# Optimization experiments

Measured on AMD Instinct MI355X. Metric: run time of the kernel, lower is better.

Reference implementation:

```python
import jax, jax.numpy as jnp
import numpy as np

LN_EPS = 1e-5
NORM_EPS = 1e-12


def entmax15_last(x):
    """Exact 1.5-entmax over the last axis (Peters & Martins sort algorithm)."""
    d = x.shape[-1]
    x = x / 2.0
    x = x - jnp.max(x, axis=-1, keepdims=True)
    xs = jnp.sort(x, axis=-1)[..., ::-1]  # descending
    k = jnp.arange(1, d + 1, dtype=x.dtype)
    mean = jnp.cumsum(xs, axis=-1) / k
    meansq = jnp.cumsum(xs * xs, axis=-1) / k
    ss = k * (meansq - jnp.square(mean))
    delta = (1.0 - ss) / k
    tau = mean - jnp.sqrt(jnp.clip(delta, 0.0))
    support = (tau <= xs).astype(jnp.int32)
    k_star = jnp.sum(support, axis=-1, keepdims=True) - 1  # last valid index
    tau_star = jnp.take_along_axis(tau, k_star, axis=-1)
    return jnp.square(jnp.maximum(x - tau_star, 0.0))


def layer_norm(x, gamma, beta):
    mu = jnp.mean(x, axis=-1, keepdims=True)
    var = jnp.mean(jnp.square(x - mu), axis=-1, keepdims=True)
    return (x - mu) / jnp.sqrt(var + LN_EPS) * gamma + beta


def setup_inputs() -> dict:
    key = jax.random.key(0)
    ks = jax.random.split(key, 4)
    B, M, N, D, T, L = 256, 64, 32, 128, 64, 128
    return {
        "x": jax.random.normal(ks[0], (B, M, D), dtype=jnp.float32),
        "route_weights": jax.random.normal(ks[1], (M, N, D, T), dtype=jnp.float32),
        "thread": jax.random.uniform(ks[2], (1, M, N), dtype=jnp.float32),
        "routing_leaves": jax.random.uniform(ks[3], (L, T), dtype=jnp.float32),
        "ln_gamma": jnp.ones((T,), dtype=jnp.float32),
        "ln_beta": jnp.zeros((T,), dtype=jnp.float32),
    }


def reference(x, route_weights, thread, routing_leaves, ln_gamma, ln_beta):
    # entmax15 over dim=-2 (the in_capsule_size axis D) of route_weights [M,N,D,T]
    w = jnp.swapaxes(route_weights, -1, -2)
    w = entmax15_last(w)
    weights = jnp.swapaxes(w, -1, -2)
    # priors: [B, M, N, T]
    priors = jnp.einsum('bmd,mndt->bmnt', x, weights)
    # routing
    leave_hash = routing_leaves / jnp.maximum(
        jnp.linalg.norm(routing_leaves, axis=-1, keepdims=True), NORM_EPS)
    votes = jax.nn.sigmoid(jnp.einsum('ld,bmnt->bmnl', leave_hash, priors)) if False else \
        jax.nn.sigmoid(jnp.einsum('ld,bmnd->bmnl', leave_hash, priors))  # [B,M,N,L]
    mean_cap = jnp.mean(votes, axis=1, keepdims=True)
    dis = jnp.mean(jnp.square(votes - mean_cap), axis=-1)  # [B,M,N]
    weight = jax.nn.relu(jnp.square(thread) - dis)
    prob = jax.nn.softmax(weight, axis=-2)  # over M (in capsules)
    next_caps = jnp.sum(prob[:, :, :, None] * priors, axis=1)  # [B,N,T]
    return layer_norm(next_caps, ln_gamma, ln_beta)
```

## Files before the change

### kernel.cpp

```cpp
#include <hip/hip_runtime.h>
#include <hip/hip_bf16.h>
#include <math.h>

#define B_ 256
#define M_ 64
#define N_ 32
#define D_ 128
#define T_ 64
#define L_ 128

typedef __attribute__((ext_vector_type(8))) short short8;
typedef __attribute__((ext_vector_type(4))) float floatx4;

__device__ __forceinline__ unsigned short f2bf(float f) {
  unsigned int u = __float_as_uint(f);
  unsigned int r = (u + 0x7fffu + ((u >> 16) & 1u)) >> 16;
  return (unsigned short)r;
}
__device__ __forceinline__ float bf2f(unsigned short s) {
  return __uint_as_float(((unsigned int)s) << 16);
}
__device__ __forceinline__ float frcp(float x) { return __builtin_amdgcn_rcpf(x); }
__device__ __forceinline__ unsigned pk2bf(float a, float b) {
  __hip_bfloat162 h = __float22bfloat162_rn(make_float2(a, b));
  unsigned u;
  __builtin_memcpy(&u, &h, 4);
  return u;
}

template <int CTRL>
__device__ __forceinline__ float dpp_f(float x) {
  return __int_as_float(__builtin_amdgcn_update_dpp(
      __float_as_int(x), __float_as_int(x), CTRL, 0xf, 0xf, false));
}
__device__ __forceinline__ float rsum16(float x) {
  x += dpp_f<0x121>(x);
  x += dpp_f<0x122>(x);
  x += dpp_f<0x124>(x);
  x += dpp_f<0x128>(x);
  return x;
}
__device__ __forceinline__ float rmax16(float x) {
  x = fmaxf(x, dpp_f<0x121>(x));
  x = fmaxf(x, dpp_f<0x122>(x));
  x = fmaxf(x, dpp_f<0x124>(x));
  x = fmaxf(x, dpp_f<0x128>(x));
  return x;
}

__global__ __launch_bounds__(256) void k_prep(const float* __restrict__ x,
                                              const float* __restrict__ leaves,
                                              unsigned short* __restrict__ xb2,
                                              unsigned short* __restrict__ lhn,
                                              const float* __restrict__ thr,
                                              float* __restrict__ thrT) {
  const int tid = threadIdx.x;
  const int bx = blockIdx.x;
  if (bx < 1024) {
    int idx = bx * 256 + tid;
    int j = idx & 15, b = (idx >> 4) & 255, m = idx >> 12;
    const float* xs = x + ((size_t)b * M_ + m) * D_ + j;
    float v[8];
#pragma unroll
    for (int i = 0; i < 8; ++i) v[i] = xs[i * 16];
    unsigned short* dst = xb2 + ((size_t)m * B_ + b) * D_ + j * 8;
    uint4 w;
    w.x = pk2bf(v[0], v[1]);
    w.y = pk2bf(v[2], v[3]);
    w.z = pk2bf(v[4], v[5]);
    w.w = pk2bf(v[6], v[7]);
    *(uint4*)dst = w;
  } else if (bx == 1024) {
    if (tid < L_) {
      const float* r = leaves + tid * T_;
      float ss = 0.f;
      for (int i = 0; i < T_; ++i) ss = fmaf(r[i], r[i], ss);
      float inv = frcp(fmaxf(sqrtf(ss), 1e-12f));
      unsigned short* o = lhn + tid * T_;
      for (int i = 0; i < T_; ++i) o[i] = f2bf(r[i] * inv);
    }
  } else {
#pragma unroll
    for (int k = 0; k < 8; ++k) {
      int idx = k * 256 + tid;
      int nn = idx >> 6, mm = idx & 63;
      thrT[idx] = thr[mm * N_ + nn];
    }
  }
}

#define BS_STRIDE 136
__global__ __launch_bounds__(256, 8) void k_wpriors(const unsigned short* __restrict__ xb2,
                                                    const float* __restrict__ rw,
                                                    unsigned short* __restrict__ priors) {
  const int m = blockIdx.x, n = blockIdx.y;
  const int tid = threadIdx.x;
  const int wid = tid >> 6, lane = tid & 63;
  const int row16 = lane & 15, quad = lane >> 4;

  __shared__ __align__(16) unsigned short Bs[64 * BS_STRIDE];

  {
    const int g = tid >> 4, j = tid & 15;
    const float* base = rw + (size_t)(m * N_ + n) * (D_ * T_) + g * 4;
    floatx4 xv[8];
#pragma unroll
    for (int i = 0; i < 8; ++i)
      xv[i] = *(const floatx4*)(base + (size_t)(i * 16 + j) * T_);

    floatx4 mx = xv[0];
#pragma unroll
    for (int i = 1; i < 8; ++i)
#pragma unroll
      for (int c = 0; c < 4; ++c) mx[c] = fmaxf(mx[c], xv[i][c]);
#pragma unroll
    for (int c = 0; c < 4; ++c) mx[c] = rmax16(mx[c]);
#pragma unroll
    for (int i = 0; i < 8; ++i)
#pragma unroll
      for (int c = 0; c < 4; ++c) xv[i][c] = (xv[i][c] - mx[c]) * 0.5f;

    floatx4 lo = (floatx4){-1.f, -1.f, -1.f, -1.f};
    floatx4 hi = (floatx4){0.f, 0.f, 0.f, 0.f};
    for (int it = 0; it < 8; ++it) {
      floatx4 tau, f = (floatx4){0.f, 0.f, 0.f, 0.f};
#pragma unroll
      for (int c = 0; c < 4; ++c) tau[c] = 0.5f * (lo[c] + hi[c]);
#pragma unroll
      for (int i = 0; i < 8; ++i)
#pragma unroll
        for (int c = 0; c < 4; ++c) {
          float u = fmaxf(xv[i][c] - tau[c], 0.0f);
          f[c] = fmaf(u, u, f[c]);
        }
#pragma unroll
      for (int c = 0; c < 4; ++c) f[c] = rsum16(f[c]);
#pragma unroll
      for (int c = 0; c < 4; ++c) {
        bool ge = f[c] >= 1.0f;
        lo[c] = ge ? tau[c] : lo[c];
        hi[c] = ge ? hi[c] : tau[c];
      }
    }
    floatx4 tau0, cnt = (floatx4){0,0,0,0}, s1 = (floatx4){0,0,0,0}, s2 = (floatx4){0,0,0,0};
#pragma unroll
    for (int c = 0; c < 4; ++c) tau0[c] = 0.5f * (lo[c] + hi[c]);
#pragma unroll
    for (int i = 0; i < 8; ++i)
#pragma unroll
      for (int c = 0; c < 4; ++c) {
        bool in = xv[i][c] > tau0[c];
        float q = in ? xv[i][c] : 0.0f;
        cnt[c] += in ? 1.0f : 0.0f;
        s1[c] += q;
        s2[c] = fmaf(q, q, s2[c]);
      }
#pragma unroll
    for (int c = 0; c < 4; ++c) {
      cnt[c] = rsum16(cnt[c]);
      s1[c] = rsum16(s1[c]);
      s2[c] = rsum16(s2[c]);
    }
    floatx4 tau;
#pragma unroll
    for (int c = 0; c < 4; ++c) {
      float rc = frcp(cnt[c]);
      float mean = s1[c] * rc;
      float ss = s2[c] - mean * s1[c];
      float delta = (1.0f - ss) * rc;
      tau[c] = mean - sqrtf(fmaxf(delta, 0.0f));
    }

#pragma unroll
    for (int c = 0; c < 4; ++c) {
      float u[8];
#pragma unroll
      for (int i = 0; i < 8; ++i) {
        float v = fmaxf(xv[i][c] - tau[c], 0.0f);
        u[i] = v * v;
      }
      uint4 w;
      w.x = pk2bf(u[0], u[1]);
      w.y = pk2bf(u[2], u[3]);
      w.z = pk2bf(u[4], u[5]);
      w.w = pk2bf(u[6], u[7]);
      *(uint4*)&Bs[(g * 4 + c) * BS_STRIDE + j * 8] = w;
    }
  }
  __syncthreads();

#pragma unroll
  for (int c = 0; c < 2; ++c) {
#pragma unroll
    for (int sub = 0; sub < 2; ++sub) {
      const int b = c * 128 + wid * 32 + sub * 16 + row16;
      const unsigned short* xptr = xb2 + ((size_t)m * B_ + b) * D_ + quad * 8;
      short8 xfr[4];
#pragma unroll
      for (int ks = 0; ks < 4; ++ks) xfr[ks] = *(const short8*)(xptr + ks * 32);

      floatx4 acc[4];
#pragma unroll
      for (int cf = 0; cf < 4; ++cf) acc[cf] = (floatx4){0.f, 0.f, 0.f, 0.f};
#pragma unroll
      for (int cf = 0; cf < 4; ++cf) {
        short8 afr[4];
#pragma unroll
        for (int ks = 0; ks < 4; ++ks)
          afr[ks] = *(const short8*)&Bs[(cf * 16 + row16) * BS_STRIDE + ks * 32 + quad * 8];
#pragma unroll
        for (int ks = 0; ks < 4; ++ks)
          acc[cf] = __builtin_amdgcn_mfma_f32_16x16x32_bf16(afr[ks], xfr[ks], acc[cf], 0, 0, 0);
      }

      unsigned X0x = pk2bf(acc[0][0], acc[0][1]), X0y = pk2bf(acc[0][2], acc[0][3]);
      unsigned X1x = pk2bf(acc[1][0], acc[1][1]), X1y = pk2bf(acc[1][2], acc[1][3]);
      unsigned X2x = pk2bf(acc[2][0], acc[2][1]), X2y = pk2bf(acc[2][2], acc[2][3]);
      unsigned X3x = pk2bf(acc[3][0], acc[3][1]), X3y = pk2bf(acc[3][2], acc[3][3]);

      const bool hi2 = (quad & 2) != 0;
      unsigned s0x = hi2 ? X0x : X2x, s0y = hi2 ? X0y : X2y;
      unsigned s1x = hi2 ? X1x : X3x, s1y = hi2 ? X1y : X3y;
      unsigned r0x = __shfl_xor(s0x, 32), r0y = __shfl_xor(s0y, 32);
      unsigned r1x = __shfl_xor(s1x, 32), r1y = __shfl_xor(s1y, 32);
      unsigned A0x = hi2 ? r0x : X0x, A0y = hi2 ? r0y : X0y;
      unsigned A1x = hi2 ? r1x : X1x, A1y = hi2 ? r1y : X1y;
      unsigned A2x = hi2 ? X2x : r0x, A2y = hi2 ? X2y : r0y;
      unsigned A3x = hi2 ? X3x : r1x, A3y = hi2 ? X3y : r1y;
      const bool odd = (quad & 1) != 0;
      unsigned t0x = odd ? A0x : A1x, t0y = odd ? A0y : A1y;
      unsigned t1x = odd ? A2x : A3x, t1y = odd ? A2y : A3y;
      unsigned u0x = __shfl_xor(t0x, 16), u0y = __shfl_xor(t0y, 16);
      unsigned u1x = __shfl_xor(t1x, 16), u1y = __shfl_xor(t1y, 16);
      uint4 w0, w1;
      w0.x = odd ? u0x : A0x;  w0.y = odd ? u0y : A0y;
      w0.z = odd ? A1x : u0x;  w0.w = odd ? A1y : u0y;
      w1.x = odd ? u1x : A2x;  w1.y = odd ? u1y : A2y;
      w1.z = odd ? A3x : u1x;  w1.w = odd ? A3y : u1y;

      unsigned short* dst = priors + (((size_t)n * B_ + b) * M_ + m) * T_ + quad * 16;
      *(uint4*)dst = w0;
      *(uint4*)(dst + 8) = w1;
    }
  }
}

__global__ __launch_bounds__(256, 4) void k_route(const unsigned short* __restrict__ priors,
                                                  const unsigned short* __restrict__ lhn,
                                                  const float* __restrict__ thrT,
                                                  const float* __restrict__ gamma,
                                                  const float* __restrict__ beta,
                                                  float* __restrict__ out) {
  const int n = blockIdx.x, g4 = blockIdx.y;
  const int tid = threadIdx.x;
  const int wid = tid >> 6, lane = tid & 63;
  const int col = lane & 15, quad = lane >> 4;

  __shared__ float probL[4][64];

  const int b = g4 * 4 + wid;

  const unsigned short* base = priors + ((size_t)n * B_ + b) * (M_ * T_);
  short8 afr[4][2];
#pragma unroll
  for (int mt = 0; mt < 4; ++mt)
#pragma unroll
    for (int ks = 0; ks < 2; ++ks)
      afr[mt][ks] = *(const short8*)(base + (mt * 16 + col) * T_ + ks * 32 + quad * 8);

  float thv = thrT[n * 64 + lane];

  float dis[4][4];
#pragma unroll
  for (int mt = 0; mt < 4; ++mt)
#pragma unroll
    for (int r = 0; r < 4; ++r) dis[mt][r] = 0.f;

#pragma unroll
  for (int s4 = 0; s4 < 4; ++s4) {
    floatx4 acc[4][2];
#pragma unroll
    for (int mt = 0; mt < 4; ++mt)
#pragma unroll
      for (int lt = 0; lt < 2; ++lt) acc[mt][lt] = (floatx4){0.f, 0.f, 0.f, 0.f};

#pragma unroll
    for (int lt = 0; lt < 2; ++lt) {
#pragma unroll
      for (int ks = 0; ks < 2; ++ks) {
        short8 bfr = *(const short8*)(lhn + (s4 * 32 + lt * 16 + col) * T_ + ks * 32 + quad * 8);
#pragma unroll
        for (int mt = 0; mt < 4; ++mt)
          acc[mt][lt] = __builtin_amdgcn_mfma_f32_16x16x32_bf16(afr[mt][ks], bfr, acc[mt][lt], 0, 0, 0);
      }
    }

#pragma unroll
    for (int mt = 0; mt < 4; ++mt)
#pragma unroll
      for (int lt = 0; lt < 2; ++lt)
#pragma unroll
        for (int r = 0; r < 4; ++r)
          acc[mt][lt][r] = frcp(1.0f + __expf(-acc[mt][lt][r]));

    float mc[2];
#pragma unroll
    for (int lt = 0; lt < 2; ++lt) {
      float s = 0.f;
#pragma unroll
      for (int mt = 0; mt < 4; ++mt)
#pragma unroll
        for (int r = 0; r < 4; ++r) s += acc[mt][lt][r];
      s += __shfl_xor(s, 16);
      s += __shfl_xor(s, 32);
      mc[lt] = s * (1.0f / 64.0f);
    }

#pragma unroll
    for (int mt = 0; mt < 4; ++mt)
#pragma unroll
      for (int r = 0; r < 4; ++r) {
        float s = 0.f;
#pragma unroll
        for (int lt = 0; lt < 2; ++lt) {
          float df = acc[mt][lt][r] - mc[lt];
          s = fmaf(df, df, s);
        }
        dis[mt][r] += s;
      }
  }

#pragma unroll
  for (int mt = 0; mt < 4; ++mt)
#pragma unroll
    for (int r = 0; r < 4; ++r) dis[mt][r] = rsum16(dis[mt][r]);

  float e[4][4];
  float mxw = 0.f;
#pragma unroll
  for (int mt = 0; mt < 4; ++mt)
#pragma unroll
    for (int r = 0; r < 4; ++r) {
      float th = __shfl(thv, mt * 16 + quad * 4 + r);
      float w = fmaxf(th * th - dis[mt][r] * (1.0f / 128.0f), 0.0f);
      e[mt][r] = w;
      mxw = fmaxf(mxw, w);
    }
  mxw = fmaxf(mxw, __shfl_xor(mxw, 16));
  mxw = fmaxf(mxw, __shfl_xor(mxw, 32));
  float ssum = 0.f;
#pragma unroll
  for (int mt = 0; mt < 4; ++mt)
#pragma unroll
    for (int r = 0; r < 4; ++r) {
      e[mt][r] = __expf(e[mt][r] - mxw);
      ssum += e[mt][r];
    }
  ssum += __shfl_xor(ssum, 16);
  ssum += __shfl_xor(ssum, 32);
  float inv = frcp(ssum);
  if (col == 0) {
#pragma unroll
    for (int mt = 0; mt < 4; ++mt)
#pragma unroll
      for (int r = 0; r < 4; ++r)
        probL[wid][mt * 16 + quad * 4 + r] = e[mt][r] * inv;
  }

  float pr[4];
#pragma unroll
  for (int mt = 0; mt < 4; ++mt) pr[mt] = probL[wid][mt * 16 + col];

  float o[2][8];
#pragma unroll
  for (int ks = 0; ks < 2; ++ks)
#pragma unroll
    for (int j = 0; j < 8; ++j) o[ks][j] = 0.f;
#pragma unroll
  for (int mt = 0; mt < 4; ++mt)
#pragma unroll
    for (int ks = 0; ks < 2; ++ks)
#pragma unroll
      for (int j = 0; j < 8; ++j)
        o[ks][j] = fmaf(pr[mt], bf2f((unsigned short)afr[mt][ks][j]), o[ks][j]);
#pragma unroll
  for (int ks = 0; ks < 2; ++ks)
#pragma unroll
    for (int j = 0; j < 8; ++j) o[ks][j] = rsum16(o[ks][j]);

  float mu = 0.f;
#pragma unroll
  for (int ks = 0; ks < 2; ++ks)
#pragma unroll
    for (int j = 0; j < 8; ++j) mu += o[ks][j];
  mu += __shfl_xor(mu, 16);
  mu += __shfl_xor(mu, 32);
  mu *= (1.0f / 64.0f);
  float var = 0.f;
#pragma unroll
  for (int ks = 0; ks < 2; ++ks)
#pragma unroll
    for (int j = 0; j < 8; ++j) {
      float d = o[ks][j] - mu;
      o[ks][j] = d;
      var = fmaf(d, d, var);
    }
  var += __shfl_xor(var, 16);
  var += __shfl_xor(var, 32);
  var *= (1.0f / 64.0f);
  float rstd = rsqrtf(var + 1e-5f);

  if (col == 0) {
    float* obase = out + ((size_t)b * N_ + n) * T_;
#pragma unroll
    for (int ks = 0; ks < 2; ++ks) {
      int tb = ks * 32 + quad * 8;
      float4 g0 = *(const float4*)(gamma + tb);
      float4 g1 = *(const float4*)(gamma + tb + 4);
      float4 b0 = *(const float4*)(beta + tb);
      float4 b1 = *(const float4*)(beta + tb + 4);
      float4 r0, r1;
      r0.x = o[ks][0] * rstd * g0.x + b0.x;
      r0.y = o[ks][1] * rstd * g0.y + b0.y;
      r0.z = o[ks][2] * rstd * g0.z + b0.z;
      r0.w = o[ks][3] * rstd * g0.w + b0.w;
      r1.x = o[ks][4] * rstd * g1.x + b1.x;
      r1.y = o[ks][5] * rstd * g1.y + b1.y;
      r1.z = o[ks][6] * rstd * g1.z + b1.z;
      r1.w = o[ks][7] * rstd * g1.w + b1.w;
      *(float4*)(obase + tb) = r0;
      *(float4*)(obase + tb + 4) = r1;
    }
  }
}

extern "C" void kernel_launch(void* const* d_in, const int* in_sizes, int n_in,
                              void* d_out, int out_size, void* d_ws, size_t ws_size,
                              hipStream_t stream) {
  const float* x = (const float*)d_in[0];
  const float* rw = (const float*)d_in[1];
  const float* thr = (const float*)d_in[2];
  const float* leaves = (const float*)d_in[3];
  const float* gamma = (const float*)d_in[4];
  const float* beta = (const float*)d_in[5];
  float* out = (float*)d_out;

  char* ws = (char*)d_ws;
  unsigned short* priors = (unsigned short*)(ws);
  unsigned short* xb2 = (unsigned short*)(ws + 67108864);
  unsigned short* lhn = (unsigned short*)(ws + 71303168);
  float* thrT = (float*)(ws + 71319552);

  hipLaunchKernelGGL(k_prep, dim3(1026), dim3(256), 0, stream, x, leaves, xb2, lhn, thr, thrT);
  hipLaunchKernelGGL(k_wpriors, dim3(64, 32), dim3(256), 0, stream, xb2, rw, priors);
  hipLaunchKernelGGL(k_route, dim3(32, 64), dim3(256), 0, stream, priors, lhn, thrT, gamma, beta, out);
}
```

Baseline: 173.1 us.

## Process two capsule columns per block, interleaving entmax with MFMA GEMM

Each k_wpriors block now handles two n indices instead of one. The global load and entmax bisection for the second weight slice are interleaved with the MFMA prior computation of the first, using a double-buffered LDS tile. The aim is to overlap the ALU-heavy entmax and memory latency with matrix-core work inside one wave. In exchange the grid is halved, launch bounds drop from 8 to 4 blocks per CU, and LDS use doubles, which lowers occupancy-based latency hiding.

```diff
diff --git a/kernel.cpp b/kernel.cpp
--- a/kernel.cpp
+++ b/kernel.cpp
@@ -90,159 +90,192 @@
 }
 
 #define BS_STRIDE 136
-__global__ __launch_bounds__(256, 8) void k_wpriors(const unsigned short* __restrict__ xb2,
+
+__device__ __forceinline__ void e_load(floatx4 xv[8], const float* __restrict__ rw,
+                                       int m, int n, int g, int j) {
+  const float* base = rw + (size_t)(m * N_ + n) * (D_ * T_) + g * 4;
+#pragma unroll
+  for (int i = 0; i < 8; ++i)
+    xv[i] = *(const floatx4*)(base + (size_t)(i * 16 + j) * T_);
+}
+
+__device__ __forceinline__ void e_init(floatx4 xv[8], floatx4& lo, floatx4& hi) {
+  floatx4 mx = xv[0];
+#pragma unroll
+  for (int i = 1; i < 8; ++i)
+#pragma unroll
+    for (int c = 0; c < 4; ++c) mx[c] = fmaxf(mx[c], xv[i][c]);
+#pragma unroll
+  for (int c = 0; c < 4; ++c) mx[c] = rmax16(mx[c]);
+#pragma unroll
+  for (int i = 0; i < 8; ++i)
+#pragma unroll
+    for (int c = 0; c < 4; ++c) xv[i][c] = (xv[i][c] - mx[c]) * 0.5f;
+  lo = (floatx4){-1.f, -1.f, -1.f, -1.f};
+  hi = (floatx4){0.f, 0.f, 0.f, 0.f};
+}
+
+__device__ __forceinline__ void e_iter(floatx4 xv[8], floatx4& lo, floatx4& hi) {
+  floatx4 tau, f = (floatx4){0.f, 0.f, 0.f, 0.f};
+#pragma unroll
+  for (int c = 0; c < 4; ++c) tau[c] = 0.5f * (lo[c] + hi[c]);
+#pragma unroll
+  for (int i = 0; i < 8; ++i)
+#pragma unroll
+    for (int c = 0; c < 4; ++c) {
+      float u = fmaxf(xv[i][c] - tau[c], 0.0f);
+      f[c] = fmaf(u, u, f[c]);
+    }
+#pragma unroll
+  for (int c = 0; c < 4; ++c) f[c] = rsum16(f[c]);
+#pragma unroll
+  for (int c = 0; c < 4; ++c) {
+    bool ge = f[c] >= 1.0f;
+    lo[c] = ge ? tau[c] : lo[c];
+    hi[c] = ge ? hi[c] : tau[c];
+  }
+}
+
+__device__ __forceinline__ void e_fin(floatx4 xv[8], floatx4 lo, floatx4 hi,
+                                      unsigned short* __restrict__ BsB, int g, int j) {
+  floatx4 tau0, cnt = (floatx4){0,0,0,0}, s1 = (floatx4){0,0,0,0}, s2 = (floatx4){0,0,0,0};
+#pragma unroll
+  for (int c = 0; c < 4; ++c) tau0[c] = 0.5f * (lo[c] + hi[c]);
+#pragma unroll
+  for (int i = 0; i < 8; ++i)
+#pragma unroll
+    for (int c = 0; c < 4; ++c) {
+      bool in = xv[i][c] > tau0[c];
+      float q = in ? xv[i][c] : 0.0f;
+      cnt[c] += in ? 1.0f : 0.0f;
+      s1[c] += q;
+      s2[c] = fmaf(q, q, s2[c]);
+    }
+#pragma unroll
+  for (int c = 0; c < 4; ++c) {
+    cnt[c] = rsum16(cnt[c]);
+    s1[c] = rsum16(s1[c]);
+    s2[c] = rsum16(s2[c]);
+  }
+  floatx4 tau;
+#pragma unroll
+  for (int c = 0; c < 4; ++c) {
+    float rc = frcp(cnt[c]);
+    float mean = s1[c] * rc;
+    float ss = s2[c] - mean * s1[c];
+    float delta = (1.0f - ss) * rc;
+    tau[c] = mean - sqrtf(fmaxf(delta, 0.0f));
+  }
+#pragma unroll
+  for (int c = 0; c < 4; ++c) {
+    float u[8];
+#pragma unroll
+    for (int i = 0; i < 8; ++i) {
+      float v = fmaxf(xv[i][c] - tau[c], 0.0f);
+      u[i] = v * v;
+    }
+    uint4 w;
+    w.x = pk2bf(u[0], u[1]);
+    w.y = pk2bf(u[2], u[3]);
+    w.z = pk2bf(u[4], u[5]);
+    w.w = pk2bf(u[6], u[7]);
+    *(uint4*)&BsB[(g * 4 + c) * BS_STRIDE + j * 8] = w;
+  }
+}
+
+__device__ __forceinline__ void g_chunk(const unsigned short* __restrict__ BsB,
+                                        const unsigned short* __restrict__ xb2m,
+                                        unsigned short* __restrict__ priors,
+                                        int m, int n, int c, int sub,
+                                        int wid, int row16, int quad) {
+  const int b = c * 128 + wid * 32 + sub * 16 + row16;
+  const unsigned short* xptr = xb2m + (size_t)b * D_ + quad * 8;
+  short8 xfr[4];
+#pragma unroll
+  for (int ks = 0; ks < 4; ++ks) xfr[ks] = *(const short8*)(xptr + ks * 32);
+
+  floatx4 acc[4];
+#pragma unroll
+  for (int cf = 0; cf < 4; ++cf) acc[cf] = (floatx4){0.f, 0.f, 0.f, 0.f};
+#pragma unroll
+  for (int cf = 0; cf < 4; ++cf) {
+    short8 afr[4];
+#pragma unroll
+    for (int ks = 0; ks < 4; ++ks)
+      afr[ks] = *(const short8*)&BsB[(cf * 16 + row16) * BS_STRIDE + ks * 32 + quad * 8];
+#pragma unroll
+    for (int ks = 0; ks < 4; ++ks)
+      acc[cf] = __builtin_amdgcn_mfma_f32_16x16x32_bf16(afr[ks], xfr[ks], acc[cf], 0, 0, 0);
+  }
+
+  unsigned X0x = pk2bf(acc[0][0], acc[0][1]), X0y = pk2bf(acc[0][2], acc[0][3]);
+  unsigned X1x = pk2bf(acc[1][0], acc[1][1]), X1y = pk2bf(acc[1][2], acc[1][3]);
+  unsigned X2x = pk2bf(acc[2][0], acc[2][1]), X2y = pk2bf(acc[2][2], acc[2][3]);
+  unsigned X3x = pk2bf(acc[3][0], acc[3][1]), X3y = pk2bf(acc[3][2], acc[3][3]);
+
+  const bool hi2 = (quad & 2) != 0;
+  unsigned s0x = hi2 ? X0x : X2x, s0y = hi2 ? X0y : X2y;
+  unsigned s1x = hi2 ? X1x : X3x, s1y = hi2 ? X1y : X3y;
+  unsigned r0x = __shfl_xor(s0x, 32), r0y = __shfl_xor(s0y, 32);
+  unsigned r1x = __shfl_xor(s1x, 32), r1y = __shfl_xor(s1y, 32);
+  unsigned A0x = hi2 ? r0x : X0x, A0y = hi2 ? r0y : X0y;
+  unsigned A1x = hi2 ? r1x : X1x, A1y = hi2 ? r1y : X1y;
+  unsigned A2x = hi2 ? X2x : r0x, A2y = hi2 ? X2y : r0y;
+  unsigned A3x = hi2 ? X3x : r1x, A3y = hi2 ? X3y : r1y;
+  const bool odd = (quad & 1) != 0;
+  unsigned t0x = odd ? A0x : A1x, t0y = odd ? A0y : A1y;
+  unsigned t1x = odd ? A2x : A3x, t1y = odd ? A2y : A3y;
+  unsigned u0x = __shfl_xor(t0x, 16), u0y = __shfl_xor(t0y, 16);
+  unsigned u1x = __shfl_xor(t1x, 16), u1y = __shfl_xor(t1y, 16);
+  uint4 w0, w1;
+  w0.x = odd ? u0x : A0x;  w0.y = odd ? u0y : A0y;
+  w0.z = odd ? A1x : u0x;  w0.w = odd ? A1y : u0y;
+  w1.x = odd ? u1x : A2x;  w1.y = odd ? u1y : A2y;
+  w1.z = odd ? A3x : u1x;  w1.w = odd ? A3y : u1y;
+
+  unsigned short* dst = priors + (((size_t)n * B_ + b) * M_ + m) * T_ + quad * 16;
+  *(uint4*)dst = w0;
+  *(uint4*)(dst + 8) = w1;
+}
+
+__global__ __launch_bounds__(256, 4) void k_wpriors(const unsigned short* __restrict__ xb2,
                                                     const float* __restrict__ rw,
                                                     unsigned short* __restrict__ priors) {
-  const int m = blockIdx.x, n = blockIdx.y;
+  const int m = blockIdx.x;
+  const int n0 = blockIdx.y * 2, n1 = n0 + 1;
   const int tid = threadIdx.x;
   const int wid = tid >> 6, lane = tid & 63;
   const int row16 = lane & 15, quad = lane >> 4;
-
-  __shared__ __align__(16) unsigned short Bs[64 * BS_STRIDE];
-
-  {
-    const int g = tid >> 4, j = tid & 15;
-    const float* base = rw + (size_t)(m * N_ + n) * (D_ * T_) + g * 4;
-    floatx4 xv[8];
-#pragma unroll
-    for (int i = 0; i < 8; ++i)
-      xv[i] = *(const floatx4*)(base + (size_t)(i * 16 + j) * T_);
-
-    floatx4 mx = xv[0];
-#pragma unroll
-    for (int i = 1; i < 8; ++i)
-#pragma unroll
-      for (int c = 0; c < 4; ++c) mx[c] = fmaxf(mx[c], xv[i][c]);
-#pragma unroll
-    for (int c = 0; c < 4; ++c) mx[c] = rmax16(mx[c]);
-#pragma unroll
-    for (int i = 0; i < 8; ++i)
-#pragma unroll
-      for (int c = 0; c < 4; ++c) xv[i][c] = (xv[i][c] - mx[c]) * 0.5f;
-
-    floatx4 lo = (floatx4){-1.f, -1.f, -1.f, -1.f};
-    floatx4 hi = (floatx4){0.f, 0.f, 0.f, 0.f};
-    for (int it = 0; it < 8; ++it) {
-      floatx4 tau, f = (floatx4){0.f, 0.f, 0.f, 0.f};
-#pragma unroll
-      for (int c = 0; c < 4; ++c) tau[c] = 0.5f * (lo[c] + hi[c]);
-#pragma unroll
-      for (int i = 0; i < 8; ++i)
-#pragma unroll
-        for (int c = 0; c < 4; ++c) {
-          float u = fmaxf(xv[i][c] - tau[c], 0.0f);
-          f[c] = fmaf(u, u, f[c]);
-        }
-#pragma unroll
-      for (int c = 0; c < 4; ++c) f[c] = rsum16(f[c]);
-#pragma unroll
-      for (int c = 0; c < 4; ++c) {
-        bool ge = f[c] >= 1.0f;
-        lo[c] = ge ? tau[c] : lo[c];
-        hi[c] = ge ? hi[c] : tau[c];
-      }
-    }
-    floatx4 tau0, cnt = (floatx4){0,0,0,0}, s1 = (floatx4){0,0,0,0}, s2 = (floatx4){0,0,0,0};
-#pragma unroll
-    for (int c = 0; c < 4; ++c) tau0[c] = 0.5f * (lo[c] + hi[c]);
-#pragma unroll
-    for (int i = 0; i < 8; ++i)
-#pragma unroll
-      for (int c = 0; c < 4; ++c) {
-        bool in = xv[i][c] > tau0[c];
-        float q = in ? xv[i][c] : 0.0f;
-        cnt[c] += in ? 1.0f : 0.0f;
-        s1[c] += q;
-        s2[c] = fmaf(q, q, s2[c]);
-      }
-#pragma unroll
-    for (int c = 0; c < 4; ++c) {
-      cnt[c] = rsum16(cnt[c]);
-      s1[c] = rsum16(s1[c]);
-      s2[c] = rsum16(s2[c]);
-    }
-    floatx4 tau;
-#pragma unroll
-    for (int c = 0; c < 4; ++c) {
-      float rc = frcp(cnt[c]);
-      float mean = s1[c] * rc;
-      float ss = s2[c] - mean * s1[c];
-      float delta = (1.0f - ss) * rc;
-      tau[c] = mean - sqrtf(fmaxf(delta, 0.0f));
-    }
-
-#pragma unroll
-    for (int c = 0; c < 4; ++c) {
-      float u[8];
-#pragma unroll
-      for (int i = 0; i < 8; ++i) {
-        float v = fmaxf(xv[i][c] - tau[c], 0.0f);
-        u[i] = v * v;
-      }
-      uint4 w;
-      w.x = pk2bf(u[0], u[1]);
-      w.y = pk2bf(u[2], u[3]);
-      w.z = pk2bf(u[4], u[5]);
-      w.w = pk2bf(u[6], u[7]);
-      *(uint4*)&Bs[(g * 4 + c) * BS_STRIDE + j * 8] = w;
-    }
-  }
+  const int g = tid >> 4, j = tid & 15;
+
+  __shared__ __align__(16) unsigned short Bs[2][64 * BS_STRIDE];
+  const unsigned short* xb2m = xb2 + (size_t)m * B_ * D_;
+
+  floatx4 xv[8], lo, hi;
+
+  e_load(xv, rw, m, n0, g, j);
+  e_init(xv, lo, hi);
+  e_iter(xv, lo, hi); e_iter(xv, lo, hi); e_iter(xv, lo, hi); e_iter(xv, lo, hi);
+  e_iter(xv, lo, hi); e_iter(xv, lo, hi); e_iter(xv, lo, hi); e_iter(xv, lo, hi);
+  e_fin(xv, lo, hi, Bs[0], g, j);
   __syncthreads();
 
-#pragma unroll
-  for (int c = 0; c < 2; ++c) {
-#pragma unroll
-    for (int sub = 0; sub < 2; ++sub) {
-      const int b = c * 128 + wid * 32 + sub * 16 + row16;
-      const unsigned short* xptr = xb2 + ((size_t)m * B_ + b) * D_ + quad * 8;
-      short8 xfr[4];
-#pragma unroll
-      for (int ks = 0; ks < 4; ++ks) xfr[ks] = *(const short8*)(xptr + ks * 32);
-
-      floatx4 acc[4];
-#pragma unroll
-      for (int cf = 0; cf < 4; ++cf) acc[cf] = (floatx4){0.f, 0.f, 0.f, 0.f};
-#pragma unroll
-      for (int cf = 0; cf < 4; ++cf) {
-        short8 afr[4];
-#pragma unroll
-        for (int ks = 0; ks < 4; ++ks)
-          afr[ks] = *(const short8*)&Bs[(cf * 16 + row16) * BS_STRIDE + ks * 32 + quad * 8];
-#pragma unroll
-        for (int ks = 0; ks < 4; ++ks)
-          acc[cf] = __builtin_amdgcn_mfma_f32_16x16x32_bf16(afr[ks], xfr[ks], acc[cf], 0, 0, 0);
-      }
-
-      unsigned X0x = pk2bf(acc[0][0], acc[0][1]), X0y = pk2bf(acc[0][2], acc[0][3]);
-      unsigned X1x = pk2bf(acc[1][0], acc[1][1]), X1y = pk2bf(acc[1][2], acc[1][3]);
-      unsigned X2x = pk2bf(acc[2][0], acc[2][1]), X2y = pk2bf(acc[2][2], acc[2][3]);
-      unsigned X3x = pk2bf(acc[3][0], acc[3][1]), X3y = pk2bf(acc[3][2], acc[3][3]);
-
-      const bool hi2 = (quad & 2) != 0;
-      unsigned s0x = hi2 ? X0x : X2x, s0y = hi2 ? X0y : X2y;
-      unsigned s1x = hi2 ? X1x : X3x, s1y = hi2 ? X1y : X3y;
-      unsigned r0x = __shfl_xor(s0x, 32), r0y = __shfl_xor(s0y, 32);
-      unsigned r1x = __shfl_xor(s1x, 32), r1y = __shfl_xor(s1y, 32);
-      unsigned A0x = hi2 ? r0x : X0x, A0y = hi2 ? r0y : X0y;
-      unsigned A1x = hi2 ? r1x : X1x, A1y = hi2 ? r1y : X1y;
-      unsigned A2x = hi2 ? X2x : r0x, A2y = hi2 ? X2y : r0y;
-      unsigned A3x = hi2 ? X3x : r1x, A3y = hi2 ? X3y : r1y;
-      const bool odd = (quad & 1) != 0;
-      unsigned t0x = odd ? A0x : A1x, t0y = odd ? A0y : A1y;
-      unsigned t1x = odd ? A2x : A3x, t1y = odd ? A2y : A3y;
-      unsigned u0x = __shfl_xor(t0x, 16), u0y = __shfl_xor(t0y, 16);
-      unsigned u1x = __shfl_xor(t1x, 16), u1y = __shfl_xor(t1y, 16);
-      uint4 w0, w1;
-      w0.x = odd ? u0x : A0x;  w0.y = odd ? u0y : A0y;
-      w0.z = odd ? A1x : u0x;  w0.w = odd ? A1y : u0y;
-      w1.x = odd ? u1x : A2x;  w1.y = odd ? u1y : A2y;
-      w1.z = odd ? A3x : u1x;  w1.w = odd ? A3y : u1y;
-
-      unsigned short* dst = priors + (((size_t)n * B_ + b) * M_ + m) * T_ + quad * 16;
-      *(uint4*)dst = w0;
-      *(uint4*)(dst + 8) = w1;
-    }
-  }
+  e_load(xv, rw, m, n1, g, j);
+  g_chunk(Bs[0], xb2m, priors, m, n0, 0, 0, wid, row16, quad);
+  g_chunk(Bs[0], xb2m, priors, m, n0, 0, 1, wid, row16, quad);
+  e_init(xv, lo, hi);
+  e_iter(xv, lo, hi); e_iter(xv, lo, hi);
+  g_chunk(Bs[0], xb2m, priors, m, n0, 1, 0, wid, row16, quad);
+  e_iter(xv, lo, hi); e_iter(xv, lo, hi);
+  g_chunk(Bs[0], xb2m, priors, m, n0, 1, 1, wid, row16, quad);
+  e_iter(xv, lo, hi); e_iter(xv, lo, hi); e_iter(xv, lo, hi); e_iter(xv, lo, hi);
+  e_fin(xv, lo, hi, Bs[1], g, j);
+  __syncthreads();
+
+  g_chunk(Bs[1], xb2m, priors, m, n1, 0, 0, wid, row16, quad);
+  g_chunk(Bs[1], xb2m, priors, m, n1, 0, 1, wid, row16, quad);
+  g_chunk(Bs[1], xb2m, priors, m, n1, 1, 0, wid, row16, quad);
+  g_chunk(Bs[1], xb2m, priors, m, n1, 1, 1, wid, row16, quad);
 }
 
 __global__ __launch_bounds__(256, 4) void k_route(const unsigned short* __restrict__ priors,
@@ -452,6 +485,6 @@
   float* thrT = (float*)(ws + 71319552);
 
   hipLaunchKernelGGL(k_prep, dim3(1026), dim3(256), 0, stream, x, leaves, xb2, lhn, thr, thrT);
-  hipLaunchKernelGGL(k_wpriors, dim3(64, 32), dim3(256), 0, stream, xb2, rw, priors);
+  hipLaunchKernelGGL(k_wpriors, dim3(64, 16), dim3(256), 0, stream, xb2, rw, priors);
   hipLaunchKernelGGL(k_route, dim3(32, 64), dim3(256), 0, stream, priors, lhn, thrT, gamma, beta, out);
 }
```

Measured after the change: 187.8 us. +8.5%, slower.
